# Performance work log

Hardware: AMD Instinct MI355X
Metric: run time of the kernel (lower is better)

Reference implementation:

```python
import jax, jax.numpy as jnp
import numpy as np
from jax import lax

B, N, D = 16, 2048, 256
H = 64  # hidden_dim
EPS = 1e-5


def zero_softmax(x, eps=EPS):
    # zeros stay exactly zero: exp(0)-1 == 0
    e = jnp.exp(x) - 1.0
    return e / (jnp.sum(e, axis=-1, keepdims=True) + eps)


def setup_inputs() -> dict:
    key = jax.random.key(0)
    ks = jax.random.split(key, 9)
    s_in = 1.0 / np.sqrt(D)
    x = jax.random.normal(ks[0], (B, N, D), dtype=jnp.float32)
    Wq = jax.random.uniform(ks[1], (D, H), jnp.float32, -s_in, s_in)
    bq = jax.random.uniform(ks[2], (H,), jnp.float32, -s_in, s_in)
    Wk = jax.random.uniform(ks[3], (D, H), jnp.float32, -s_in, s_in)
    bk = jax.random.uniform(ks[4], (H,), jnp.float32, -s_in, s_in)
    Wv = jax.random.uniform(ks[5], (D, H), jnp.float32, -s_in, s_in)
    bv = jax.random.uniform(ks[6], (H,), jnp.float32, -s_in, s_in)
    s_c = 1.0 / 3.0  # conv fan_in = 1*3*3 = 9
    conv_w = jax.random.uniform(ks[7], (1, 1, 3, 3), jnp.float32, -s_c, s_c)
    conv_b = jax.random.uniform(ks[8], (1,), jnp.float32, -s_c, s_c)
    return {"x": x, "Wq": Wq, "bq": bq, "Wk": Wk, "bk": bk,
            "Wv": Wv, "bv": bv, "conv_w": conv_w, "conv_b": conv_b}


def reference(x, Wq, bq, Wk, bk, Wv, bv, conv_w, conv_b):
    scale = H ** (-0.5)
    q = jnp.einsum('bnd,dh->bnh', x, Wq) + bq
    k = jnp.einsum('bnd,dh->bnh', x, Wk) + bk
    v = jnp.einsum('bnd,dh->bnh', x, Wv) + bv
    A_dense = jnp.einsum('bnh,bmh->bnm', q, k) * scale  # [B, N, N]
    A_in = A_dense[:, None, :, :]  # [B, 1, N, N]
    A_conv = lax.conv_general_dilated(
        A_in, conv_w, window_strides=(1, 1), padding='SAME',
        dimension_numbers=('NCHW', 'OIHW', 'NCHW')) + conv_b[None, :, None, None]
    A_conv = jax.nn.sigmoid(A_conv)[:, 0, :, :]
    A_sparse = jax.nn.relu(A_dense - A_conv)
    A_norm = zero_softmax(A_sparse)
    return jnp.einsum('bnm,bmh->bnh', A_norm, v)
```

## Files before the change

kernel.cpp:

```cpp
#include <hip/hip_runtime.h>
#include <hip/hip_bf16.h>

typedef __bf16 bf16_t;
typedef __bf16 bf16x8 __attribute__((ext_vector_type(8)));
typedef float  floatx4 __attribute__((ext_vector_type(4)));

#define BQ 16
#define NTOK 2048
#define DIM 256
#define HD 64

__global__ __launch_bounds__(256) void k_prep(const float* __restrict__ Wq,
                                              const float* __restrict__ Wk,
                                              const float* __restrict__ Wv,
                                              bf16_t* __restrict__ wt,
                                              float* __restrict__ outz,
                                              float* __restrict__ rsz) {
    int o = blockIdx.x * 256 + threadIdx.x;
    if (o < 49152) {
        int w = o >> 14;
        int r = o & 16383;
        int h = r >> 8;
        int d = r & 255;
        const float* W = (w == 0) ? Wq : ((w == 1) ? Wk : Wv);
        wt[o] = (bf16_t)W[d * 64 + h];
    }
    float4 z = make_float4(0.f, 0.f, 0.f, 0.f);
    for (int u = o; u < 532480; u += 262144) {
        if (u < 524288) ((float4*)outz)[u] = z;
        else            ((float4*)rsz)[u - 524288] = z;
    }
}

#define XS 264
__global__ __launch_bounds__(256) void k_qkv(const float* __restrict__ x,
                                             const bf16_t* __restrict__ wt,
                                             const float* __restrict__ bq,
                                             const float* __restrict__ bk,
                                             const float* __restrict__ bv,
                                             bf16_t* __restrict__ qb,
                                             bf16_t* __restrict__ kb,
                                             bf16_t* __restrict__ vt) {
    __shared__ bf16_t x_ls[64 * XS];
    __shared__ bf16_t vt_ls[64 * 72];

    int b  = blockIdx.x >> 5;
    int t0 = (blockIdx.x & 31) << 6;
    int t  = threadIdx.x;
    int lane = t & 63;
    int w    = t >> 6;
    int m_   = lane & 15;
    int q4   = lane >> 4;

    for (int tau = t; tau < 4096; tau += 256) {
        int row = tau >> 6, ch = tau & 63;
        float4 v = ((const float4*)x)[(size_t)(b * NTOK + t0 + row) * 64 + ch];
        bf16_t tmp[4] = {(bf16_t)v.x, (bf16_t)v.y, (bf16_t)v.z, (bf16_t)v.w};
        *(uint2*)(&x_ls[row * XS + ch * 4]) = *(uint2*)tmp;
    }
    __syncthreads();

    for (int wi = 0; wi < 3; ++wi) {
        const bf16_t* wtw = wt + wi * 16384;
        floatx4 acc[4];
        #pragma unroll
        for (int mt = 0; mt < 4; ++mt) acc[mt] = floatx4{0.f, 0.f, 0.f, 0.f};

        #pragma unroll
        for (int ks = 0; ks < 8; ++ks) {
            bf16x8 bfrag = *(const bf16x8*)(wtw + (16 * w + m_) * 256 + ks * 32 + q4 * 8);
            #pragma unroll
            for (int mt = 0; mt < 4; ++mt) {
                bf16x8 afrag = *(const bf16x8*)(&x_ls[(16 * mt + m_) * XS + ks * 32 + q4 * 8]);
                acc[mt] = __builtin_amdgcn_mfma_f32_16x16x32_bf16(afrag, bfrag, acc[mt], 0, 0, 0);
            }
        }
        const float* bias_p = (wi == 0) ? bq : ((wi == 1) ? bk : bv);
        float bias = bias_p[16 * w + m_];
        float scale = (wi == 0) ? 0.125f : 1.0f;

        if (wi < 2) {
            bf16_t* dst = (wi == 0) ? qb : kb;
            #pragma unroll
            for (int mt = 0; mt < 4; ++mt)
                #pragma unroll
                for (int r = 0; r < 4; ++r) {
                    int tok = t0 + 16 * mt + 4 * q4 + r;
                    dst[(size_t)(b * NTOK + tok) * 64 + 16 * w + m_] = (bf16_t)((acc[mt][r] + bias) * scale);
                }
        } else {
            #pragma unroll
            for (int mt = 0; mt < 4; ++mt)
                #pragma unroll
                for (int r = 0; r < 4; ++r)
                    vt_ls[(16 * w + m_) * 72 + 16 * mt + 4 * q4 + r] = (bf16_t)(acc[mt][r] + bias);
            __syncthreads();
            for (int tau = t; tau < 512; tau += 256) {
                int h = tau >> 3, ch = tau & 7;
                uint4 val = *(const uint4*)(&vt_ls[h * 72 + ch * 8]);
                *(uint4*)(vt + (size_t)(b * 64 + h) * NTOK + t0 + ch * 8) = val;
            }
        }
    }
}

#define SA 52
#define SP 72
#define RINT 46
#define NIT_C 15
__global__ __launch_bounds__(256) void k_attn(const bf16_t* __restrict__ qb,
                                              const bf16_t* __restrict__ kb,
                                              const bf16_t* __restrict__ vt,
                                              const float* __restrict__ conv_w,
                                              const float* __restrict__ conv_b,
                                              float* __restrict__ outp,
                                              float* __restrict__ rsg) {
    __shared__ bf16_t q_ls[48 * SP];
    __shared__ bf16_t k_ls[48 * SP];
    __shared__ bf16_t v_ls[64 * SP];
    __shared__ float  A_ls[48 * SA];
    __shared__ bf16_t p_ls[48 * SP];

    int b    = blockIdx.z;
    int r0   = blockIdx.x * RINT;
    int ch0  = blockIdx.y * NIT_C;
    int t = threadIdx.x, lane = t & 63, w = t >> 6;
    int m_ = lane & 15, q4 = lane >> 4;

    const uint* vt32 = (const uint*)vt + (size_t)b * 64 * 1024;

    int vh[6], vc[6];
    #pragma unroll
    for (int j = 0; j < 6; ++j) { int tau = t + 256 * j; vh[j] = tau / 23; vc[j] = tau % 23; }

    float cw[9];
    #pragma unroll
    for (int i = 0; i < 9; ++i) cw[i] = conv_w[i];
    float cb = conv_b[0];

    uint4 kreg[2];
    uint  vreg[6];
    auto prefetch = [&](int c0) {
        {
            int row = t >> 3, ch = t & 7;
            int g = c0 - 1 + row;
            uint4 val = make_uint4(0u, 0u, 0u, 0u);
            if (g >= 0 && g < NTOK)
                val = *(const uint4*)(kb + (size_t)(b * NTOK + g) * 64 + ch * 8);
            kreg[0] = val;
        }
        if (t < 128) {
            int row = (t + 256) >> 3, ch = t & 7;
            int g = c0 - 1 + row;
            uint4 val = make_uint4(0u, 0u, 0u, 0u);
            if (g >= 0 && g < NTOK)
                val = *(const uint4*)(kb + (size_t)(b * NTOK + g) * 64 + ch * 8);
            kreg[1] = val;
        }
        #pragma unroll
        for (int j = 0; j < 6; ++j) {
            if (t + 256 * j < 1472) {
                int n = c0 + 2 * vc[j];
                uint val = 0u;
                if (n < NTOK) val = vt32[vh[j] * 1024 + (n >> 1)];
                vreg[j] = val;
            }
        }
    };

    prefetch(ch0 * RINT);

    for (int u = t; u < 1728; u += 256) ((uint*)p_ls)[u] = 0u;
    for (int u = t; u < 1152; u += 256) {
        int h = u / 18, c = 46 + u % 18;
        v_ls[h * SP + c] = (bf16_t)0.f;
    }
    if (t < 192) A_ls[(t >> 2) * SA + 48 + (t & 3)] = 0.f;
    for (int tau = t; tau < 384; tau += 256) {
        int row = tau >> 3, ch = tau & 7;
        int g = r0 - 1 + row;
        uint4 val = make_uint4(0u, 0u, 0u, 0u);
        if (g >= 0 && g < NTOK)
            val = *(const uint4*)(qb + (size_t)(b * NTOK + g) * 64 + ch * 8);
        *(uint4*)(&q_ls[row * SP + ch * 8]) = val;
    }

    floatx4 accO[3];
    #pragma unroll
    for (int ti = 0; ti < 3; ++ti) accO[ti] = floatx4{0.f, 0.f, 0.f, 0.f};
    float rs[3] = {0.f, 0.f, 0.f};

    for (int it = 0; it < NIT_C; ++it) {
        {
            int row = t >> 3, ch = t & 7;
            *(uint4*)(&k_ls[row * SP + ch * 8]) = kreg[0];
            if (t < 128) {
                int row1 = (t + 256) >> 3;
                *(uint4*)(&k_ls[row1 * SP + ch * 8]) = kreg[1];
            }
            #pragma unroll
            for (int j = 0; j < 6; ++j)
                if (t + 256 * j < 1472)
                    *(uint*)(&v_ls[vh[j] * SP + 2 * vc[j]]) = vreg[j];
        }
        __syncthreads();

        for (int T = w; T < 9; T += 4) {
            int ti = T / 3, tj = T % 3;
            floatx4 a = floatx4{0.f, 0.f, 0.f, 0.f};
            #pragma unroll
            for (int ks = 0; ks < 2; ++ks) {
                bf16x8 af = *(const bf16x8*)(&q_ls[(16 * ti + m_) * SP + ks * 32 + q4 * 8]);
                bf16x8 bf = *(const bf16x8*)(&k_ls[(16 * tj + m_) * SP + ks * 32 + q4 * 8]);
                a = __builtin_amdgcn_mfma_f32_16x16x32_bf16(af, bf, a, 0, 0, 0);
            }
            #pragma unroll
            for (int r = 0; r < 4; ++r)
                A_ls[(16 * ti + 4 * q4 + r) * SA + 16 * tj + m_] = a[r];
        }
        __syncthreads();

        if (it + 1 < NIT_C) prefetch((ch0 + it + 1) * RINT);

        #pragma unroll
        for (int round = 0; round < 3; ++round) {
            int idx = t + (round << 8);
            if (idx < 552) {
                int i = idx / 12 + 1;
                int g = idx - (i - 1) * 12;
                const float* base = &A_ls[(i - 1) * SA + 4 * g];
                float a0[6], a1[6], a2[6];
                *(float4*)(a0) = *(const float4*)(base);
                *(float2*)(a0 + 4) = *(const float2*)(base + 4);
                *(float4*)(a1) = *(const float4*)(base + SA);
                *(float2*)(a1 + 4) = *(const float2*)(base + SA + 4);
                *(float4*)(a2) = *(const float4*)(base + 2 * SA);
                *(float2*)(a2 + 4) = *(const float2*)(base + 2 * SA + 4);
                float esum = 0.f;
                bf16_t quad[4];
                #pragma unroll
                for (int x = 0; x < 4; ++x) {
                    float conv = cb
                        + cw[0] * a0[x] + cw[1] * a0[x + 1] + cw[2] * a0[x + 2]
                        + cw[3] * a1[x] + cw[4] * a1[x + 1] + cw[5] * a1[x + 2]
                        + cw[6] * a2[x] + cw[7] * a2[x + 1] + cw[8] * a2[x + 2];
                    float sig = __builtin_amdgcn_rcpf(1.f + __expf(-conv));
                    float s = fmaxf(a1[x + 1] - sig, 0.f);
                    float ev = __expf(s) - 1.f;
                    if (4 * g + x > 45) ev = 0.f;
                    quad[x] = (bf16_t)ev;
                    esum += ev;
                }
                rs[round] += esum;
                *(uint2*)(&p_ls[i * SP + 4 * g]) = *(uint2*)quad;
            }
        }
        __syncthreads();

        #pragma unroll
        for (int ks = 0; ks < 2; ++ks) {
            bf16x8 bf = *(const bf16x8*)(&v_ls[(16 * w + m_) * SP + ks * 32 + q4 * 8]);
            #pragma unroll
            for (int ti = 0; ti < 3; ++ti) {
                bf16x8 af = *(const bf16x8*)(&p_ls[(16 * ti + m_) * SP + ks * 32 + q4 * 8]);
                accO[ti] = __builtin_amdgcn_mfma_f32_16x16x32_bf16(af, bf, accO[ti], 0, 0, 0);
            }
        }
        __syncthreads();
    }

    float* sc = A_ls;
    sc[t * 3 + 0] = rs[0];
    sc[t * 3 + 1] = rs[1];
    sc[t * 3 + 2] = rs[2];
    __syncthreads();
    if (t < RINT) {
        float s = 0.f;
        #pragma unroll
        for (int j = 0; j < 12; ++j) {
            int idx = 12 * t + j;
            s += sc[(idx & 255) * 3 + (idx >> 8)];
        }
        int grow = r0 + t;
        if (grow < NTOK) atomicAdd(&rsg[b * NTOK + grow], s);
    }

    #pragma unroll
    for (int ti = 0; ti < 3; ++ti) {
        #pragma unroll
        for (int r = 0; r < 4; ++r) {
            int i = 16 * ti + 4 * q4 + r;
            int grow = r0 + i - 1;
            if (i >= 1 && i < 47 && grow < NTOK)
                atomicAdd(&outp[((size_t)(b * NTOK + grow) << 6) + 16 * w + m_], accO[ti][r]);
        }
    }
}

__global__ __launch_bounds__(256) void k_norm(float* __restrict__ out,
                                              const float* __restrict__ rsg) {
    int gid = blockIdx.x * 256 + threadIdx.x;
    float4 o = ((float4*)out)[gid];
    float d = rsg[gid >> 4] + 1e-5f;
    float inv = 1.f / d;
    o.x *= inv; o.y *= inv; o.z *= inv; o.w *= inv;
    ((float4*)out)[gid] = o;
}

extern "C" void kernel_launch(void* const* d_in, const int* in_sizes, int n_in,
                              void* d_out, int out_size, void* d_ws, size_t ws_size,
                              hipStream_t stream) {
    const float* x  = (const float*)d_in[0];
    const float* Wq = (const float*)d_in[1];
    const float* bq = (const float*)d_in[2];
    const float* Wk = (const float*)d_in[3];
    const float* bk = (const float*)d_in[4];
    const float* Wv = (const float*)d_in[5];
    const float* bv = (const float*)d_in[6];
    const float* cw = (const float*)d_in[7];
    const float* cb = (const float*)d_in[8];
    float* out = (float*)d_out;

    char* ws = (char*)d_ws;
    bf16_t* wt = (bf16_t*)ws;
    bf16_t* qb = (bf16_t*)(ws + 98304);
    bf16_t* kb = (bf16_t*)(ws + 98304 + 4194304);
    bf16_t* vt = (bf16_t*)(ws + 98304 + 8388608);
    float*  rsg = (float*)(ws + 98304 + 12582912);

    k_prep<<<dim3(1024), dim3(256), 0, stream>>>(Wq, Wk, Wv, wt, out, rsg);
    k_qkv<<<dim3(512), dim3(256), 0, stream>>>(x, wt, bq, bk, bv, qb, kb, vt);
    k_attn<<<dim3(45, 3, BQ), dim3(256), 0, stream>>>(qb, kb, vt, cw, cb, out, rsg);
    k_norm<<<dim3(2048), dim3(256), 0, stream>>>(out, rsg);
}
```

Measured before the change: 226.8 us.

## Keep QK scores in registers and compute conv stencil via lane shuffles

The attention kernel drops the shared-memory staging of Q, K, V and the score tile. Q fragments now live in registers for the whole block, and K/V fragments are loaded straight from global memory into registers with one-iteration prefetch. The 3x3 convolution is evaluated on the MFMA accumulator layout using cross-lane shuffles plus a small shared seam buffer for the edges between warps. Column tiles become 62 wide (64 computed, rim columns masked), and the column range is split into chunks of 12 iterations across blockIdx.y. Separately, the QKV projection moves to 32-token tiles so twice as many blocks launch. The cost is more register pressure and shuffle traffic, and correctness now depends on the overlapping tile and seam indexing being exact.

```diff
diff --git a/kernel.cpp b/kernel.cpp
--- a/kernel.cpp
+++ b/kernel.cpp
@@ -7,8 +7,6 @@
 
 #define BQ 16
 #define NTOK 2048
-#define DIM 256
-#define HD 64
 
 __global__ __launch_bounds__(256) void k_prep(const float* __restrict__ Wq,
                                               const float* __restrict__ Wk,
@@ -33,6 +31,7 @@
 }
 
 #define XS 264
+#define VS 40
 __global__ __launch_bounds__(256) void k_qkv(const float* __restrict__ x,
                                              const bf16_t* __restrict__ wt,
                                              const float* __restrict__ bq,
@@ -41,18 +40,18 @@
                                              bf16_t* __restrict__ qb,
                                              bf16_t* __restrict__ kb,
                                              bf16_t* __restrict__ vt) {
-    __shared__ bf16_t x_ls[64 * XS];
-    __shared__ bf16_t vt_ls[64 * 72];
-
-    int b  = blockIdx.x >> 5;
-    int t0 = (blockIdx.x & 31) << 6;
+    __shared__ bf16_t x_ls[32 * XS];
+    __shared__ bf16_t vt_ls[64 * VS];
+
+    int b  = blockIdx.x >> 6;
+    int t0 = (blockIdx.x & 63) << 5;
     int t  = threadIdx.x;
     int lane = t & 63;
     int w    = t >> 6;
     int m_   = lane & 15;
     int q4   = lane >> 4;
 
-    for (int tau = t; tau < 4096; tau += 256) {
+    for (int tau = t; tau < 2048; tau += 256) {
         int row = tau >> 6, ch = tau & 63;
         float4 v = ((const float4*)x)[(size_t)(b * NTOK + t0 + row) * 64 + ch];
         bf16_t tmp[4] = {(bf16_t)v.x, (bf16_t)v.y, (bf16_t)v.z, (bf16_t)v.w};
@@ -62,15 +61,15 @@
 
     for (int wi = 0; wi < 3; ++wi) {
         const bf16_t* wtw = wt + wi * 16384;
-        floatx4 acc[4];
-        #pragma unroll
-        for (int mt = 0; mt < 4; ++mt) acc[mt] = floatx4{0.f, 0.f, 0.f, 0.f};
+        floatx4 acc[2];
+        #pragma unroll
+        for (int mt = 0; mt < 2; ++mt) acc[mt] = floatx4{0.f, 0.f, 0.f, 0.f};
 
         #pragma unroll
         for (int ks = 0; ks < 8; ++ks) {
             bf16x8 bfrag = *(const bf16x8*)(wtw + (16 * w + m_) * 256 + ks * 32 + q4 * 8);
             #pragma unroll
-            for (int mt = 0; mt < 4; ++mt) {
+            for (int mt = 0; mt < 2; ++mt) {
                 bf16x8 afrag = *(const bf16x8*)(&x_ls[(16 * mt + m_) * XS + ks * 32 + q4 * 8]);
                 acc[mt] = __builtin_amdgcn_mfma_f32_16x16x32_bf16(afrag, bfrag, acc[mt], 0, 0, 0);
             }
@@ -82,7 +81,7 @@
         if (wi < 2) {
             bf16_t* dst = (wi == 0) ? qb : kb;
             #pragma unroll
-            for (int mt = 0; mt < 4; ++mt)
+            for (int mt = 0; mt < 2; ++mt)
                 #pragma unroll
                 for (int r = 0; r < 4; ++r) {
                     int tok = t0 + 16 * mt + 4 * q4 + r;
@@ -90,24 +89,24 @@
                 }
         } else {
             #pragma unroll
-            for (int mt = 0; mt < 4; ++mt)
+            for (int mt = 0; mt < 2; ++mt)
                 #pragma unroll
                 for (int r = 0; r < 4; ++r)
-                    vt_ls[(16 * w + m_) * 72 + 16 * mt + 4 * q4 + r] = (bf16_t)(acc[mt][r] + bias);
+                    vt_ls[(16 * w + m_) * VS + 16 * mt + 4 * q4 + r] = (bf16_t)(acc[mt][r] + bias);
             __syncthreads();
-            for (int tau = t; tau < 512; tau += 256) {
-                int h = tau >> 3, ch = tau & 7;
-                uint4 val = *(const uint4*)(&vt_ls[h * 72 + ch * 8]);
+            {
+                int h = t >> 2, ch = t & 3;
+                uint4 val = *(const uint4*)(&vt_ls[h * VS + ch * 8]);
                 *(uint4*)(vt + (size_t)(b * 64 + h) * NTOK + t0 + ch * 8) = val;
             }
         }
     }
 }
 
-#define SA 52
-#define SP 72
-#define RINT 46
-#define NIT_C 15
+#define PS 72
+#define NITC 34
+#define CHUNK 12
+#define GX 45
 __global__ __launch_bounds__(256) void k_attn(const bf16_t* __restrict__ qb,
                                               const bf16_t* __restrict__ kb,
                                               const bf16_t* __restrict__ vt,
@@ -115,186 +114,195 @@
                                               const float* __restrict__ conv_b,
                                               float* __restrict__ outp,
                                               float* __restrict__ rsg) {
-    __shared__ bf16_t q_ls[48 * SP];
-    __shared__ bf16_t k_ls[48 * SP];
-    __shared__ bf16_t v_ls[64 * SP];
-    __shared__ float  A_ls[48 * SA];
-    __shared__ bf16_t p_ls[48 * SP];
-
-    int b    = blockIdx.z;
-    int r0   = blockIdx.x * RINT;
-    int ch0  = blockIdx.y * NIT_C;
+    __shared__ __align__(16) char smem[12288];
+    bf16_t* pls    = (bf16_t*)smem;
+    float*  seamG0 = (float*)(smem + 6912);
+    float*  seamG2 = (float*)(smem + 7680);
+    float*  scr    = (float*)smem;
+
+    int b  = blockIdx.z;
+    int bx = blockIdx.x;
+    int it0   = blockIdx.y * CHUNK;
+    int itEnd = (it0 + CHUNK < NITC) ? (it0 + CHUNK) : NITC;
     int t = threadIdx.x, lane = t & 63, w = t >> 6;
     int m_ = lane & 15, q4 = lane >> 4;
-
-    const uint* vt32 = (const uint*)vt + (size_t)b * 64 * 1024;
-
-    int vh[6], vc[6];
-    #pragma unroll
-    for (int j = 0; j < 6; ++j) { int tau = t + 256 * j; vh[j] = tau / 23; vc[j] = tau % 23; }
 
     float cw[9];
     #pragma unroll
     for (int i = 0; i < 9; ++i) cw[i] = conv_w[i];
     float cb = conv_b[0];
 
-    uint4 kreg[2];
-    uint  vreg[6];
-    auto prefetch = [&](int c0) {
-        {
-            int row = t >> 3, ch = t & 7;
-            int g = c0 - 1 + row;
-            uint4 val = make_uint4(0u, 0u, 0u, 0u);
-            if (g >= 0 && g < NTOK)
-                val = *(const uint4*)(kb + (size_t)(b * NTOK + g) * 64 + ch * 8);
-            kreg[0] = val;
-        }
-        if (t < 128) {
-            int row = (t + 256) >> 3, ch = t & 7;
-            int g = c0 - 1 + row;
-            uint4 val = make_uint4(0u, 0u, 0u, 0u);
-            if (g >= 0 && g < NTOK)
-                val = *(const uint4*)(kb + (size_t)(b * NTOK + g) * 64 + ch * 8);
-            kreg[1] = val;
-        }
-        #pragma unroll
-        for (int j = 0; j < 6; ++j) {
-            if (t + 256 * j < 1472) {
-                int n = c0 + 2 * vc[j];
-                uint val = 0u;
-                if (n < NTOK) val = vt32[vh[j] * 1024 + (n >> 1)];
-                vreg[j] = val;
-            }
-        }
-    };
-
-    prefetch(ch0 * RINT);
-
-    for (int u = t; u < 1728; u += 256) ((uint*)p_ls)[u] = 0u;
-    for (int u = t; u < 1152; u += 256) {
-        int h = u / 18, c = 46 + u % 18;
-        v_ls[h * SP + c] = (bf16_t)0.f;
-    }
-    if (t < 192) A_ls[(t >> 2) * SA + 48 + (t & 3)] = 0.f;
-    for (int tau = t; tau < 384; tau += 256) {
-        int row = tau >> 3, ch = tau & 7;
-        int g = r0 - 1 + row;
-        uint4 val = make_uint4(0u, 0u, 0u, 0u);
-        if (g >= 0 && g < NTOK)
-            val = *(const uint4*)(qb + (size_t)(b * NTOK + g) * 64 + ch * 8);
-        *(uint4*)(&q_ls[row * SP + ch * 8]) = val;
-    }
+    bf16x8 qf[3][2];
+    {
+        int tokq = 46 * bx - 1 + m_;
+        #pragma unroll
+        for (int si = 0; si < 3; ++si) {
+            int tok = tokq + 16 * si;
+            bool ok = (tok >= 0) && (tok < NTOK);
+            #pragma unroll
+            for (int ks = 0; ks < 2; ++ks) {
+                bf16x8 v = {};
+                if (ok) v = *(const bf16x8*)(qb + ((size_t)(b * NTOK + tok)) * 64 + ks * 32 + q4 * 8);
+                qf[si][ks] = v;
+            }
+        }
+    }
+
+    bool rimcol = ((w == 0) && (m_ == 0)) || ((w == 3) && (m_ == 15));
 
     floatx4 accO[3];
     #pragma unroll
-    for (int ti = 0; ti < 3; ++ti) accO[ti] = floatx4{0.f, 0.f, 0.f, 0.f};
-    float rs[3] = {0.f, 0.f, 0.f};
-
-    for (int it = 0; it < NIT_C; ++it) {
-        {
-            int row = t >> 3, ch = t & 7;
-            *(uint4*)(&k_ls[row * SP + ch * 8]) = kreg[0];
-            if (t < 128) {
-                int row1 = (t + 256) >> 3;
-                *(uint4*)(&k_ls[row1 * SP + ch * 8]) = kreg[1];
-            }
-            #pragma unroll
-            for (int j = 0; j < 6; ++j)
-                if (t + 256 * j < 1472)
-                    *(uint*)(&v_ls[vh[j] * SP + 2 * vc[j]]) = vreg[j];
+    for (int si = 0; si < 3; ++si) accO[si] = floatx4{0.f, 0.f, 0.f, 0.f};
+    float rs[3][4] = {};
+
+    const bf16_t* kbb = kb + (size_t)b * NTOK * 64;
+    const bf16_t* vtb = vt + (size_t)b * 64 * NTOK;
+    size_t vrow = (size_t)(16 * w + m_) * NTOK;
+
+    bf16x8 kf[2], vf[2];
+    auto load_kv = [&](int it, bf16x8* kd, bf16x8* vd) {
+        int fs = 62 * it - 2;
+        int tok = fs + 16 * w + m_;
+        bool ok = (tok >= 0) && (tok < NTOK);
+        #pragma unroll
+        for (int ks = 0; ks < 2; ++ks) {
+            bf16x8 v = {};
+            if (ok) v = *(const bf16x8*)(kbb + (size_t)tok * 64 + ks * 32 + q4 * 8);
+            kd[ks] = v;
+        }
+        #pragma unroll
+        for (int ks = 0; ks < 2; ++ks) {
+            int col = fs + 32 * ks + 8 * q4;
+            if (col < 0 || col > NTOK - 8) {
+                bf16x8 v = {};
+                #pragma unroll
+                for (int j = 0; j < 8; ++j) {
+                    int tk = col + j;
+                    if (tk >= 0 && tk < NTOK) v[j] = vtb[vrow + tk];
+                }
+                vd[ks] = v;
+            } else {
+                vd[ks] = *(const bf16x8*)(vtb + vrow + col);
+            }
+        }
+    };
+    load_kv(it0, kf, vf);
+
+    for (int it = it0; it < itEnd; ++it) {
+        floatx4 Cq[3];
+        #pragma unroll
+        for (int si = 0; si < 3; ++si) {
+            floatx4 c = floatx4{0.f, 0.f, 0.f, 0.f};
+            #pragma unroll
+            for (int ks = 0; ks < 2; ++ks)
+                c = __builtin_amdgcn_mfma_f32_16x16x32_bf16(qf[si][ks], kf[ks], c, 0, 0, 0);
+            Cq[si] = c;
+        }
+
+        float cp[3][4];
+        #pragma unroll
+        for (int si = 0; si < 3; ++si) {
+            float a_up = __shfl(Cq[si][3], lane - 16);
+            float b_up = (si > 0) ? __shfl(Cq[si - 1][3], lane + 48) : 0.f;
+            float c_dn = __shfl(Cq[si][0], lane + 16);
+            float d_dn = (si < 2) ? __shfl(Cq[si + 1][0], lane - 48) : 0.f;
+            float up[4], dn[4];
+            up[0] = (q4 > 0) ? a_up : b_up;
+            up[1] = Cq[si][0]; up[2] = Cq[si][1]; up[3] = Cq[si][2];
+            dn[0] = Cq[si][1]; dn[1] = Cq[si][2]; dn[2] = Cq[si][3];
+            dn[3] = (q4 < 3) ? c_dn : d_dn;
+
+            float G0[4], G1[4], G2[4];
+            #pragma unroll
+            for (int r = 0; r < 4; ++r) {
+                float cu = Cq[si][r];
+                G0[r] = cw[0] * up[r] + cw[3] * cu + cw[6] * dn[r];
+                G1[r] = cw[1] * up[r] + cw[4] * cu + cw[7] * dn[r];
+                G2[r] = cw[2] * up[r] + cw[5] * cu + cw[8] * dn[r];
+            }
+            #pragma unroll
+            for (int r = 0; r < 4; ++r) {
+                float e0 = __shfl(G0[r], lane - 1);
+                float e2 = __shfl(G2[r], lane + 1);
+                cp[si][r] = G1[r] + ((m_ >= 1) ? e0 : 0.f) + ((m_ <= 14) ? e2 : 0.f);
+            }
+            if (m_ == 15) {
+                float4 tv = make_float4(G0[0], G0[1], G0[2], G0[3]);
+                *(float4*)&seamG0[w * 48 + 16 * si + 4 * q4] = tv;
+            }
+            if (m_ == 0) {
+                float4 tv = make_float4(G2[0], G2[1], G2[2], G2[3]);
+                *(float4*)&seamG2[w * 48 + 16 * si + 4 * q4] = tv;
+            }
         }
         __syncthreads();
 
-        for (int T = w; T < 9; T += 4) {
-            int ti = T / 3, tj = T % 3;
-            floatx4 a = floatx4{0.f, 0.f, 0.f, 0.f};
-            #pragma unroll
-            for (int ks = 0; ks < 2; ++ks) {
-                bf16x8 af = *(const bf16x8*)(&q_ls[(16 * ti + m_) * SP + ks * 32 + q4 * 8]);
-                bf16x8 bf = *(const bf16x8*)(&k_ls[(16 * tj + m_) * SP + ks * 32 + q4 * 8]);
-                a = __builtin_amdgcn_mfma_f32_16x16x32_bf16(af, bf, a, 0, 0, 0);
-            }
-            #pragma unroll
-            for (int r = 0; r < 4; ++r)
-                A_ls[(16 * ti + 4 * q4 + r) * SA + 16 * tj + m_] = a[r];
+        bf16x8 kn[2] = {}, vn[2] = {};
+        bool pf = (it + 1 < itEnd);
+        if (pf) load_kv(it + 1, kn, vn);
+
+        #pragma unroll
+        for (int si = 0; si < 3; ++si) {
+            if (m_ == 0 && w > 0) {
+                float4 s0 = *(const float4*)&seamG0[(w - 1) * 48 + 16 * si + 4 * q4];
+                cp[si][0] += s0.x; cp[si][1] += s0.y; cp[si][2] += s0.z; cp[si][3] += s0.w;
+            }
+            if (m_ == 15 && w < 3) {
+                float4 s2 = *(const float4*)&seamG2[(w + 1) * 48 + 16 * si + 4 * q4];
+                cp[si][0] += s2.x; cp[si][1] += s2.y; cp[si][2] += s2.z; cp[si][3] += s2.w;
+            }
+            #pragma unroll
+            for (int r = 0; r < 4; ++r) {
+                float conv = cp[si][r] + cb;
+                float sig = __builtin_amdgcn_rcpf(1.f + __expf(-conv));
+                float s = fmaxf(Cq[si][r] - sig, 0.f);
+                float ev = __expf(s) - 1.f;
+                if (rimcol) ev = 0.f;
+                rs[si][r] += ev;
+                pls[(16 * si + 4 * q4 + r) * PS + 16 * w + m_] = (bf16_t)ev;
+            }
         }
         __syncthreads();
 
-        if (it + 1 < NIT_C) prefetch((ch0 + it + 1) * RINT);
-
-        #pragma unroll
-        for (int round = 0; round < 3; ++round) {
-            int idx = t + (round << 8);
-            if (idx < 552) {
-                int i = idx / 12 + 1;
-                int g = idx - (i - 1) * 12;
-                const float* base = &A_ls[(i - 1) * SA + 4 * g];
-                float a0[6], a1[6], a2[6];
-                *(float4*)(a0) = *(const float4*)(base);
-                *(float2*)(a0 + 4) = *(const float2*)(base + 4);
-                *(float4*)(a1) = *(const float4*)(base + SA);
-                *(float2*)(a1 + 4) = *(const float2*)(base + SA + 4);
-                *(float4*)(a2) = *(const float4*)(base + 2 * SA);
-                *(float2*)(a2 + 4) = *(const float2*)(base + 2 * SA + 4);
-                float esum = 0.f;
-                bf16_t quad[4];
-                #pragma unroll
-                for (int x = 0; x < 4; ++x) {
-                    float conv = cb
-                        + cw[0] * a0[x] + cw[1] * a0[x + 1] + cw[2] * a0[x + 2]
-                        + cw[3] * a1[x] + cw[4] * a1[x + 1] + cw[5] * a1[x + 2]
-                        + cw[6] * a2[x] + cw[7] * a2[x + 1] + cw[8] * a2[x + 2];
-                    float sig = __builtin_amdgcn_rcpf(1.f + __expf(-conv));
-                    float s = fmaxf(a1[x + 1] - sig, 0.f);
-                    float ev = __expf(s) - 1.f;
-                    if (4 * g + x > 45) ev = 0.f;
-                    quad[x] = (bf16_t)ev;
-                    esum += ev;
-                }
-                rs[round] += esum;
-                *(uint2*)(&p_ls[i * SP + 4 * g]) = *(uint2*)quad;
-            }
-        }
-        __syncthreads();
-
-        #pragma unroll
-        for (int ks = 0; ks < 2; ++ks) {
-            bf16x8 bf = *(const bf16x8*)(&v_ls[(16 * w + m_) * SP + ks * 32 + q4 * 8]);
-            #pragma unroll
-            for (int ti = 0; ti < 3; ++ti) {
-                bf16x8 af = *(const bf16x8*)(&p_ls[(16 * ti + m_) * SP + ks * 32 + q4 * 8]);
-                accO[ti] = __builtin_amdgcn_mfma_f32_16x16x32_bf16(af, bf, accO[ti], 0, 0, 0);
-            }
-        }
-        __syncthreads();
-    }
-
-    float* sc = A_ls;
-    sc[t * 3 + 0] = rs[0];
-    sc[t * 3 + 1] = rs[1];
-    sc[t * 3 + 2] = rs[2];
+        #pragma unroll
+        for (int ks = 0; ks < 2; ++ks)
+            #pragma unroll
+            for (int si = 0; si < 3; ++si) {
+                bf16x8 af = *(const bf16x8*)(pls + (16 * si + m_) * PS + ks * 32 + q4 * 8);
+                accO[si] = __builtin_amdgcn_mfma_f32_16x16x32_bf16(af, vf[ks], accO[si], 0, 0, 0);
+            }
+        if (pf) {
+            #pragma unroll
+            for (int ks = 0; ks < 2; ++ks) { kf[ks] = kn[ks]; vf[ks] = vn[ks]; }
+        }
+    }
+
     __syncthreads();
-    if (t < RINT) {
-        float s = 0.f;
-        #pragma unroll
-        for (int j = 0; j < 12; ++j) {
-            int idx = 12 * t + j;
-            s += sc[(idx & 255) * 3 + (idx >> 8)];
-        }
-        int grow = r0 + t;
-        if (grow < NTOK) atomicAdd(&rsg[b * NTOK + grow], s);
-    }
-
     #pragma unroll
-    for (int ti = 0; ti < 3; ++ti) {
+    for (int si = 0; si < 3; ++si)
+        #pragma unroll
+        for (int r = 0; r < 4; ++r)
+            scr[(16 * si + 4 * q4 + r) * 64 + 16 * w + m_] = rs[si][r];
+    __syncthreads();
+    if (t < 46) {
+        int grow = 46 * bx + t;
+        if (grow < NTOK) {
+            const float4* p4 = (const float4*)(scr + (t + 1) * 64);
+            float s = 0.f;
+            #pragma unroll
+            for (int j = 0; j < 16; ++j) { float4 v = p4[j]; s += v.x + v.y + v.z + v.w; }
+            atomicAdd(&rsg[b * NTOK + grow], s);
+        }
+    }
+    #pragma unroll
+    for (int si = 0; si < 3; ++si)
         #pragma unroll
         for (int r = 0; r < 4; ++r) {
-            int i = 16 * ti + 4 * q4 + r;
-            int grow = r0 + i - 1;
-            if (i >= 1 && i < 47 && grow < NTOK)
-                atomicAdd(&outp[((size_t)(b * NTOK + grow) << 6) + 16 * w + m_], accO[ti][r]);
-        }
-    }
+            int f = 16 * si + 4 * q4 + r;
+            int grow = 46 * bx - 1 + f;
+            if (f >= 1 && f < 47 && grow < NTOK)
+                atomicAdd(outp + ((size_t)(b * NTOK + grow)) * 64 + 16 * w + m_, accO[si][r]);
+        }
 }
 
 __global__ __launch_bounds__(256) void k_norm(float* __restrict__ out,
@@ -329,7 +337,7 @@
     float*  rsg = (float*)(ws + 98304 + 12582912);
 
     k_prep<<<dim3(1024), dim3(256), 0, stream>>>(Wq, Wk, Wv, wt, out, rsg);
-    k_qkv<<<dim3(512), dim3(256), 0, stream>>>(x, wt, bq, bk, bv, qb, kb, vt);
-    k_attn<<<dim3(45, 3, BQ), dim3(256), 0, stream>>>(qb, kb, vt, cw, cb, out, rsg);
+    k_qkv<<<dim3(1024), dim3(256), 0, stream>>>(x, wt, bq, bk, bv, qb, kb, vt);
+    k_attn<<<dim3(GX, 3, BQ), dim3(256), 0, stream>>>(qb, kb, vt, cw, cb, out, rsg);
     k_norm<<<dim3(2048), dim3(256), 0, stream>>>(out, rsg);
 }
```

Result: slower. 240.0 us (+5.8%).
